# Kernel tuning notes

Measured on AMD Instinct MI355X. Metric: run time of the kernel, lower is better.

The kernel has to match this reference:

```python
import jax, jax.numpy as jnp
import numpy as np

DEPTH, DIM, HEADS, MLP_HID, POS_DIM, PROJ_DIM, NCLS, INP = 5, 128, 8, 256, 128, 128, 1000, 35
EPS = 1e-5

def _ln(x, g, b):
    m = x.mean(-1, keepdims=True)
    v = ((x - m) ** 2).mean(-1, keepdims=True)
    return (x - m) / jnp.sqrt(v + EPS) * g + b

def _gelu(x):
    return jax.nn.gelu(x, approximate=False)  # torch nn.GELU default (erf)

def setup_inputs() -> dict:
    key = jax.random.key(0)
    ks = iter(jax.random.split(key, 80))
    nxt = lambda: next(ks)
    B, N = 8, 1024
    w = lambda *s: (jax.random.normal(nxt(), s, jnp.float32) / np.sqrt(s[-2]).astype(np.float32))
    z = lambda *s: jnp.zeros(s, jnp.float32)
    o = lambda *s: jnp.ones(s, jnp.float32)
    node_feat = jax.random.normal(nxt(), (B, N, 3), jnp.float32)
    a = (jax.random.uniform(nxt(), (B, N, N)) < 0.01).astype(jnp.float32)
    adj = jnp.maximum(a, a.transpose(0, 2, 1))  # symmetric 0/1 adjacency
    lapl = jax.random.normal(nxt(), (B, N, 32), jnp.float32) * 0.1
    d = dict(
        node_feat=node_feat, adj=adj, lapl=lapl,
        cls_token=jax.random.normal(nxt(), (1, 1, DIM), jnp.float32),
        pe_w1=w(INP, 2 * INP), pe_b1=z(2 * INP),
        pe_w2=w(2 * INP, 2 * INP), pe_b2=z(2 * INP),
        pe_w3=w(2 * INP, 2 * INP), pe_b3=z(2 * INP),
        pe_lng=o(2 * INP), pe_lnb=z(2 * INP),
        pe_w4=w(2 * INP, POS_DIM), pe_b4=z(POS_DIM),
        blk_ln1_g=o(DEPTH, DIM), blk_ln1_b=z(DEPTH, DIM),
        blk_qkv_w=w(DEPTH, DIM, 3 * HEADS * DIM),
        blk_proj_w=w(DEPTH, HEADS * DIM, DIM), blk_proj_b=z(DEPTH, DIM),
        blk_gamma_w=jax.random.uniform(nxt(), (DEPTH, DIM, 2), jnp.float32) * 0.01,
        blk_gamma_b=z(DEPTH, 2),
        blk_ln2_g=o(DEPTH, DIM), blk_ln2_b=z(DEPTH, DIM),
        blk_mlp_w1=w(DEPTH, DIM, MLP_HID), blk_mlp_b1=z(DEPTH, MLP_HID),
        blk_mlp_w2=w(DEPTH, MLP_HID, DIM), blk_mlp_b2=z(DEPTH, DIM),
        head_lng=o(DIM), head_lnb=z(DIM), head_w=w(DIM, DIM), head_b=z(DIM),
        proj_w1=w(DIM, PROJ_DIM), proj_b1=z(PROJ_DIM),
        proj_w2=w(PROJ_DIM, PROJ_DIM), proj_b2=z(PROJ_DIM),
        proj_w3=w(PROJ_DIM, PROJ_DIM), proj_b3=z(PROJ_DIM),
        proj_lng=o(PROJ_DIM), proj_lnb=z(PROJ_DIM),
        proj_w4=w(PROJ_DIM, NCLS), proj_b4=z(NCLS),
    )
    return d

def reference(node_feat, adj, lapl, cls_token, pe_w1, pe_b1, pe_w2, pe_b2, pe_w3, pe_b3,
              pe_lng, pe_lnb, pe_w4, pe_b4, blk_ln1_g, blk_ln1_b, blk_qkv_w, blk_proj_w,
              blk_proj_b, blk_gamma_w, blk_gamma_b, blk_ln2_g, blk_ln2_b, blk_mlp_w1,
              blk_mlp_b1, blk_mlp_w2, blk_mlp_b2, head_lng, head_lnb, head_w, head_b,
              proj_w1, proj_b1, proj_w2, proj_b2, proj_w3, proj_b3, proj_lng, proj_lnb,
              proj_w4, proj_b4):
    B, N, _ = node_feat.shape
    M = N + 1
    # positional-encoding MLP on concatenated [node_feat | lapl] (inp_dim = 35)
    x = jnp.concatenate([node_feat, lapl], axis=2)
    x = _gelu(x @ pe_w1 + pe_b1)
    x = _gelu(x @ pe_w2 + pe_b2)
    x = _gelu(x @ pe_w3 + pe_b3)
    x = _ln(x, pe_lng, pe_lnb) @ pe_w4 + pe_b4  # [B,N,DIM]
    x = jnp.concatenate([jnp.broadcast_to(cls_token, (B, 1, DIM)), x], axis=1)  # [B,M,DIM]
    # adjacency with cls row/col, adj_cls[:,0,0] = 1
    adj_cls = jnp.zeros((B, M, M), x.dtype).at[:, 0, 0].set(1.0).at[:, 1:, 1:].set(adj)
    scale = DIM ** (-0.5)
    for i in range(DEPTH):
        h = _ln(x, blk_ln1_g[i], blk_ln1_b[i])
        qkv = (h @ blk_qkv_w[i]).reshape(B, M, 3, HEADS, DIM).transpose(2, 0, 3, 1, 4)
        q, k, v = qkv[0], qkv[1], qkv[2]  # each [B,H,M,D]
        attn = jnp.einsum('bhnd,bhmd->bhnm', q, k) * scale
        gamma = jnp.exp(h @ blk_gamma_w[i] + blk_gamma_b[i])  # [B,M,2], use_exp=True
        attn = gamma[:, None, :, 0:1] * attn + gamma[:, None, :, 1:2] * adj_cls[:, None]
        attn = jax.nn.softmax(attn, axis=-1)
        o = jnp.einsum('bhnm,bhmd->bhnd', attn, v).transpose(0, 2, 1, 3).reshape(B, M, HEADS * DIM)
        x = o @ blk_proj_w[i] + blk_proj_b[i] + h  # residual from normed input (as in source)
        h2 = _ln(x, blk_ln2_g[i], blk_ln2_b[i])
        x = _gelu(h2 @ blk_mlp_w1[i] + blk_mlp_b1[i]) @ blk_mlp_w2[i] + blk_mlp_b2[i] + h2
    c = x[:, 0]
    c = _ln(c, head_lng, head_lnb) @ head_w + head_b  # mlp_head
    p = _gelu(c @ proj_w1 + proj_b1)
    p = _gelu(p @ proj_w2 + proj_b2)
    p = _gelu(p @ proj_w3 + proj_b3)
    p = _ln(p, proj_lng, proj_lnb) @ proj_w4 + proj_b4
    return (c, p)
```

## Files before the change

kernel.cpp:

```cpp
#include <hip/hip_runtime.h>
#include <hip/hip_bf16.h>
#include <math.h>

#define NB 8
#define NSEQ 1024
#define M_ 1025
#define ROWS (NB * M_)
#define DIMC 128
#define NHEADS 8
#define QKV3 3072
#define PEROWS (NB * NSEQ)
#define ACS 1088

typedef __attribute__((ext_vector_type(8))) short bf16x8;
typedef __attribute__((ext_vector_type(4))) float f32x4;

__device__ __forceinline__ float gelu_f(float x) {
  return 0.5f * x * (1.f + erff(x * 0.70710678118654752440f));
}

__device__ __forceinline__ unsigned short f2bf(float f) {
  __hip_bfloat16 h = __float2bfloat16(f);
  return *reinterpret_cast<unsigned short*>(&h);
}

__device__ __forceinline__ float bf2f(unsigned short u) {
  union { unsigned int i; float f; } c;
  c.i = ((unsigned int)u) << 16;
  return c.f;
}

__global__ __launch_bounds__(128) void pe_fused_k(
    const float* __restrict__ nf, const float* __restrict__ lp,
    const float* __restrict__ w1, const float* __restrict__ b1,
    const float* __restrict__ w2, const float* __restrict__ b2,
    const float* __restrict__ w3, const float* __restrict__ b3,
    const float* __restrict__ lng, const float* __restrict__ lnb,
    const float* __restrict__ w4, const float* __restrict__ b4,
    float* __restrict__ x)
{
  __shared__ float sA[16][36];
  __shared__ float sB[16][72];
  __shared__ float sC[16][72];
  const int tid = threadIdx.x;
  const int r0 = blockIdx.x * 16;

  for (int i = tid; i < 16 * 35; i += 128) {
    const int r = i / 35, c = i - r * 35;
    const int gr = r0 + r;
    sA[r][c] = (c < 3) ? nf[(size_t)gr * 3 + c] : lp[(size_t)gr * 32 + (c - 3)];
  }
  __syncthreads();
  if (tid < 70) {
    float acc[16];
#pragma unroll
    for (int r = 0; r < 16; ++r) acc[r] = b1[tid];
    for (int k = 0; k < 35; ++k) {
      const float wv = w1[k * 70 + tid];
#pragma unroll
      for (int r = 0; r < 16; ++r) acc[r] = fmaf(sA[r][k], wv, acc[r]);
    }
#pragma unroll
    for (int r = 0; r < 16; ++r) sB[r][tid] = gelu_f(acc[r]);
  }
  __syncthreads();
  if (tid < 70) {
    float acc[16];
#pragma unroll
    for (int r = 0; r < 16; ++r) acc[r] = b2[tid];
    for (int k = 0; k < 70; ++k) {
      const float wv = w2[k * 70 + tid];
#pragma unroll
      for (int r = 0; r < 16; ++r) acc[r] = fmaf(sB[r][k], wv, acc[r]);
    }
#pragma unroll
    for (int r = 0; r < 16; ++r) sC[r][tid] = gelu_f(acc[r]);
  }
  __syncthreads();
  if (tid < 70) {
    float acc[16];
#pragma unroll
    for (int r = 0; r < 16; ++r) acc[r] = b3[tid];
    for (int k = 0; k < 70; ++k) {
      const float wv = w3[k * 70 + tid];
#pragma unroll
      for (int r = 0; r < 16; ++r) acc[r] = fmaf(sC[r][k], wv, acc[r]);
    }
#pragma unroll
    for (int r = 0; r < 16; ++r) sB[r][tid] = gelu_f(acc[r]);
  }
  __syncthreads();
  if (tid < 16) {
    float m = 0.f;
    for (int d = 0; d < 70; ++d) m += sB[tid][d];
    m *= (1.f / 70.f);
    float v = 0.f;
    for (int d = 0; d < 70; ++d) { const float t = sB[tid][d] - m; v += t * t; }
    const float inv = rsqrtf(v * (1.f / 70.f) + 1e-5f);
    for (int d = 0; d < 70; ++d) sB[tid][d] = (sB[tid][d] - m) * inv * lng[d] + lnb[d];
  }
  __syncthreads();
  {
    float acc[16];
#pragma unroll
    for (int r = 0; r < 16; ++r) acc[r] = b4[tid];
    for (int k = 0; k < 70; ++k) {
      const float wv = w4[k * 128 + tid];
#pragma unroll
      for (int r = 0; r < 16; ++r) acc[r] = fmaf(sB[r][k], wv, acc[r]);
    }
#pragma unroll
    for (int r = 0; r < 16; ++r) {
      const int gr = r0 + r;
      x[(size_t)(gr + gr / 1024 + 1) * DIMC + tid] = acc[r];
    }
  }
}

template<int ACT, int OBF, int RES>
__global__ __launch_bounds__(256) void mgemm_k(
    const unsigned short* __restrict__ Xb, const unsigned short* __restrict__ Wt,
    const float* __restrict__ bias, const float* __restrict__ res,
    void* __restrict__ outp, int rows, int K, int N)
{
  __shared__ unsigned short sX[64][72];
  __shared__ unsigned short sW[64][72];
  const int tid = threadIdx.x;
  const int w = tid >> 6, lane = tid & 63;
  const int col = lane & 15, quad = lane >> 4;
  const int r0 = blockIdx.x * 64, n0 = blockIdx.y * 64;
  const int lr = tid >> 2, lc = tid & 3;
  const int xrow = min(r0 + lr, rows - 1);
  const unsigned short* xsrc = Xb + (size_t)xrow * K + lc * 8;
  const unsigned short* wsrc = Wt + (size_t)(n0 + lr) * K + lc * 8;

  f32x4 acc[4];
#pragma unroll
  for (int t = 0; t < 4; ++t) acc[t] = (f32x4){0.f, 0.f, 0.f, 0.f};

  for (int k0 = 0; k0 < K; k0 += 64) {
    __syncthreads();
    *(uint4*)&sX[lr][lc * 8]      = *(const uint4*)(xsrc + k0);
    *(uint4*)&sX[lr][lc * 8 + 32] = *(const uint4*)(xsrc + k0 + 32);
    *(uint4*)&sW[lr][lc * 8]      = *(const uint4*)(wsrc + k0);
    *(uint4*)&sW[lr][lc * 8 + 32] = *(const uint4*)(wsrc + k0 + 32);
    __syncthreads();
    const bf16x8 aX0 = *(const bf16x8*)&sX[w * 16 + col][quad * 8];
    const bf16x8 aX1 = *(const bf16x8*)&sX[w * 16 + col][32 + quad * 8];
#pragma unroll
    for (int t = 0; t < 4; ++t) {
      const bf16x8 bW0 = *(const bf16x8*)&sW[t * 16 + col][quad * 8];
      const bf16x8 bW1 = *(const bf16x8*)&sW[t * 16 + col][32 + quad * 8];
      acc[t] = __builtin_amdgcn_mfma_f32_16x16x32_bf16(aX0, bW0, acc[t], 0, 0, 0);
      acc[t] = __builtin_amdgcn_mfma_f32_16x16x32_bf16(aX1, bW1, acc[t], 0, 0, 0);
    }
  }
  const int gr_base = r0 + w * 16 + quad * 4;
#pragma unroll
  for (int t = 0; t < 4; ++t) {
    const int n = n0 + t * 16 + col;
    const float bv = bias ? bias[n] : 0.f;
#pragma unroll
    for (int r = 0; r < 4; ++r) {
      const int gr = gr_base + r;
      if (gr < rows) {
        float v = acc[t][r] + bv;
        if (ACT) v = gelu_f(v);
        if (RES) v += res[(size_t)gr * N + n];
        if (OBF) ((unsigned short*)outp)[(size_t)gr * N + n] = f2bf(v);
        else     ((float*)outp)[(size_t)gr * N + n] = v;
      }
    }
  }
}

template<int OBF, int VT>
__global__ __launch_bounds__(256) void mgemm128_k(
    const unsigned short* __restrict__ Xb, const unsigned short* __restrict__ Wt,
    const float* __restrict__ bias, void* __restrict__ outp,
    unsigned short* __restrict__ vtp, int rows, int K, int N)
{
  __shared__ unsigned short sX[128][72];
  __shared__ unsigned short sW[128][72];
  const int tid = threadIdx.x;
  const int w = tid >> 6, lane = tid & 63;
  const int col = lane & 15, quad = lane >> 4;
  const int wr = w >> 1, wc = w & 1;
  const int r0 = blockIdx.x * 128, n0 = blockIdx.y * 128;

  f32x4 acc[4][4];
#pragma unroll
  for (int i = 0; i < 4; ++i)
#pragma unroll
    for (int j = 0; j < 4; ++j) acc[i][j] = (f32x4){0.f, 0.f, 0.f, 0.f};

  for (int k0 = 0; k0 < K; k0 += 64) {
    __syncthreads();
#pragma unroll
    for (int l = 0; l < 4; ++l) {
      const int idx = l * 256 + tid;
      const int row = idx >> 3, c = idx & 7;
      const int xrow = min(r0 + row, rows - 1);
      *(uint4*)&sX[row][c * 8] = *(const uint4*)(Xb + (size_t)xrow * K + k0 + c * 8);
      *(uint4*)&sW[row][c * 8] = *(const uint4*)(Wt + (size_t)(n0 + row) * K + k0 + c * 8);
    }
    __syncthreads();
    bf16x8 aX[4][2];
#pragma unroll
    for (int i = 0; i < 4; ++i) {
      aX[i][0] = *(const bf16x8*)&sX[wr * 64 + i * 16 + col][quad * 8];
      aX[i][1] = *(const bf16x8*)&sX[wr * 64 + i * 16 + col][32 + quad * 8];
    }
#pragma unroll
    for (int j = 0; j < 4; ++j) {
      const bf16x8 b0 = *(const bf16x8*)&sW[wc * 64 + j * 16 + col][quad * 8];
      const bf16x8 b1 = *(const bf16x8*)&sW[wc * 64 + j * 16 + col][32 + quad * 8];
#pragma unroll
      for (int i = 0; i < 4; ++i) {
        acc[i][j] = __builtin_amdgcn_mfma_f32_16x16x32_bf16(aX[i][0], b0, acc[i][j], 0, 0, 0);
        acc[i][j] = __builtin_amdgcn_mfma_f32_16x16x32_bf16(aX[i][1], b1, acc[i][j], 0, 0, 0);
      }
    }
  }
  const bool dovt = VT && (n0 >= 2048);
#pragma unroll
  for (int i = 0; i < 4; ++i) {
    const int gr_base = r0 + wr * 64 + i * 16 + quad * 4;
    int bb[4], mm[4];
    if (dovt) {
#pragma unroll
      for (int r = 0; r < 4; ++r) {
        const int gr = gr_base + r;
        bb[r] = gr / 1025;
        mm[r] = gr - bb[r] * 1025;
      }
    }
#pragma unroll
    for (int j = 0; j < 4; ++j) {
      const int n = n0 + wc * 64 + j * 16 + col;
      const float bv = bias ? bias[n] : 0.f;
      const int hh = (n - 2048) >> 7;
      const int d  = (n - 2048) & 127;
#pragma unroll
      for (int r = 0; r < 4; ++r) {
        const int gr = gr_base + r;
        if (gr < rows) {
          const float v = acc[i][j][r] + bv;
          const unsigned short bf = f2bf(v);
          if (OBF) ((unsigned short*)outp)[(size_t)gr * N + n] = bf;
          else     ((float*)outp)[(size_t)gr * N + n] = v;
          if (dovt) vtp[(((size_t)(bb[r] * NHEADS + hh) * DIMC + d) * ACS) + mm[r]] = bf;
        }
      }
    }
  }
}

__global__ __launch_bounds__(256) void ln_rows_k(
    const float* __restrict__ in, float* __restrict__ out,
    unsigned short* __restrict__ outb,
    const float* __restrict__ g, const float* __restrict__ b,
    const float* __restrict__ gw, const float* __restrict__ gb,
    float* __restrict__ gamout, int rows, int D)
{
  const int wv = (blockIdx.x * blockDim.x + threadIdx.x) >> 6;
  const int lane = threadIdx.x & 63;
  if (wv >= rows) return;
  const float* r = in + (size_t)wv * D;
  float s = 0.f;
  for (int d = lane; d < D; d += 64) s += r[d];
  for (int off = 32; off; off >>= 1) s += __shfl_down(s, off);
  const float mean = __shfl(s, 0) / (float)D;
  float v = 0.f;
  for (int d = lane; d < D; d += 64) { float t = r[d] - mean; v += t * t; }
  for (int off = 32; off; off >>= 1) v += __shfl_down(v, off);
  const float inv = rsqrtf(__shfl(v, 0) / (float)D + 1e-5f);
  float* orow = out + (size_t)wv * D;
  float a0 = 0.f, a1 = 0.f;
  for (int d = lane; d < D; d += 64) {
    const float o = (r[d] - mean) * inv * g[d] + b[d];
    orow[d] = o;
    if (outb) outb[(size_t)wv * D + d] = f2bf(o);
    if (gw) { a0 = fmaf(o, gw[2 * d], a0); a1 = fmaf(o, gw[2 * d + 1], a1); }
  }
  if (gw) {
    for (int off = 32; off; off >>= 1) { a0 += __shfl_down(a0, off); a1 += __shfl_down(a1, off); }
    if (lane == 0) {
      gamout[(size_t)wv * 2 + 0] = expf(a0 + gb[0]);
      gamout[(size_t)wv * 2 + 1] = expf(a1 + gb[1]);
    }
  }
}

__global__ __launch_bounds__(256) void adjp_k(const float* __restrict__ adj,
                                              unsigned long long* __restrict__ adjp)
{
  const int n = blockIdx.x;
  const int b = blockIdx.y;
  const int wv = threadIdx.x >> 6, lane = threadIdx.x & 63;
  for (int w = wv; w < 17; w += 4) {
    const int m = w * 64 + lane;
    float av = 0.f;
    if (n == 0) av = (m == 0) ? 1.f : 0.f;
    else if (m >= 1 && m <= NSEQ) av = adj[((size_t)b * NSEQ + (n - 1)) * NSEQ + (m - 1)];
    const unsigned long long mask = __ballot(av != 0.f);
    if (lane == 0) adjp[((size_t)b * M_ + n) * 17 + w] = mask;
  }
}

__global__ void wtrans_k(const float* __restrict__ W, unsigned short* __restrict__ Wt,
                         int K, int N)
{
  __shared__ float t[32][33];
  const int k0 = blockIdx.x * 32, n0 = blockIdx.y * 32;
  const float* Wd = W + (size_t)blockIdx.z * K * N;
  unsigned short* Wtd = Wt + (size_t)blockIdx.z * K * N;
  for (int i = threadIdx.y; i < 32; i += 8)
    t[i][threadIdx.x] = Wd[(size_t)(k0 + i) * N + n0 + threadIdx.x];
  __syncthreads();
  for (int i = threadIdx.y; i < 32; i += 8)
    Wtd[(size_t)(n0 + i) * K + k0 + threadIdx.x] = f2bf(t[threadIdx.x][i]);
}

__global__ __launch_bounds__(256) void attn_mfma_k(
    const unsigned short* __restrict__ qkv, const float* __restrict__ gamma,
    const unsigned long long* __restrict__ adjp, const unsigned short* __restrict__ vt,
    unsigned short* __restrict__ o)
{
  __shared__ unsigned short sK[64][136];
  __shared__ unsigned short sVt[128][72];
  __shared__ unsigned short sP[64][72];

  const int hh = blockIdx.x, qt = blockIdx.y, b = blockIdx.z;
  const int tid = threadIdx.x;
  const int w = tid >> 6;
  const int lane = tid & 63;
  const int col = lane & 15;
  const int quad = lane >> 4;
  const int n0 = qt * 64;
  const int qbase = n0 + w * 16;
  const float scale = 0.088388347648318447f;

  bf16x8 aQ[4];
  {
    const int qrow = min(qbase + col, 1024);
    const unsigned short* qp = qkv + ((size_t)(b * M_ + qrow)) * QKV3 + hh * DIMC + quad * 8;
#pragma unroll
    for (int c = 0; c < 4; ++c) aQ[c] = *(const bf16x8*)(qp + c * 32);
  }
  float g0[4], g1[4];
  size_t adjo[4];
#pragma unroll
  for (int r = 0; r < 4; ++r) {
    const int nc = min(qbase + quad * 4 + r, 1024);
    g0[r] = gamma[(size_t)(b * M_ + nc) * 2 + 0] * scale;
    g1[r] = gamma[(size_t)(b * M_ + nc) * 2 + 1];
    adjo[r] = ((size_t)b * M_ + nc) * 17;
  }

  float l_i[4] = {0.f, 0.f, 0.f, 0.f};
  f32x4 Oacc[8];
#pragma unroll
  for (int t = 0; t < 8; ++t) Oacc[t] = (f32x4){0.f, 0.f, 0.f, 0.f};

  const size_t vtbase = ((size_t)(b * NHEADS + hh)) * DIMC * ACS;

  for (int kt = 0; kt < 17; ++kt) {
    const int m0 = kt * 64;
    __syncthreads();
#pragma unroll
    for (int l = 0; l < 4; ++l) {
      const int idx = l * 256 + tid;
      {
        const int m = idx >> 4, c = idx & 15;
        const int gm = m0 + m;
        uint4 kv = make_uint4(0u, 0u, 0u, 0u);
        if (gm < M_) kv = *(const uint4*)(qkv + ((size_t)(b * M_ + gm)) * QKV3 + 1024 + hh * DIMC + c * 8);
        *(uint4*)&sK[m][c * 8] = kv;
      }
      {
        const int d = idx >> 3, mc = idx & 7;
        const uint4 vv = *(const uint4*)(vt + vtbase + (size_t)d * ACS + m0 + mc * 8);
        const int swc = mc ^ ((d >> 3) & 7);
        *(uint4*)&sVt[d][swc * 8] = vv;
      }
    }
    __syncthreads();

    unsigned long long mk[4];
#pragma unroll
    for (int r = 0; r < 4; ++r) mk[r] = adjp[adjo[r] + kt];

    f32x4 Sacc[4];
#pragma unroll
    for (int t = 0; t < 4; ++t) Sacc[t] = (f32x4){0.f, 0.f, 0.f, 0.f};
#pragma unroll
    for (int t = 0; t < 4; ++t) {
#pragma unroll
      for (int c = 0; c < 4; ++c) {
        const bf16x8 bK = *(const bf16x8*)&sK[t * 16 + col][c * 32 + quad * 8];
        Sacc[t] = __builtin_amdgcn_mfma_f32_16x16x32_bf16(aQ[c], bK, Sacc[t], 0, 0, 0);
      }
    }

#pragma unroll
    for (int t = 0; t < 4; ++t) {
      const int m = m0 + t * 16 + col;
      const bool mv = (m < M_);
      const int chb = t * 2 + (col >> 3);
      const int sh = t * 16 + col;
#pragma unroll
      for (int r = 0; r < 4; ++r) {
        const float bias = ((mk[r] >> sh) & 1ull) ? g1[r] : 0.f;
        const float s = fmaf(g0[r], Sacc[t][r], bias);
        const float pv = mv ? __expf(s) : 0.f;
        l_i[r] += pv;
        const int ql = w * 16 + quad * 4 + r;
        sP[ql][((chb ^ (ql & 7)) * 8) + (col & 7)] = f2bf(pv);
      }
    }

#pragma unroll
    for (int ch = 0; ch < 2; ++ch) {
      const int r0a = w * 16 + col;
      const bf16x8 aP = *(const bf16x8*)&sP[r0a][(((ch * 4 + quad) ^ (col & 7)) * 8)];
#pragma unroll
      for (int t = 0; t < 8; ++t) {
        const int pc = (ch * 4 + quad) ^ ((t * 2 + (col >> 3)) & 7);
        const bf16x8 bV = *(const bf16x8*)&sVt[t * 16 + col][pc * 8];
        Oacc[t] = __builtin_amdgcn_mfma_f32_16x16x32_bf16(aP, bV, Oacc[t], 0, 0, 0);
      }
    }
  }

#pragma unroll
  for (int r = 0; r < 4; ++r) {
    float s = l_i[r];
    s += __shfl_xor(s, 1);
    s += __shfl_xor(s, 2);
    s += __shfl_xor(s, 4);
    s += __shfl_xor(s, 8);
    const int n = qbase + quad * 4 + r;
    if (n < M_) {
      const float invl = 1.f / s;
      unsigned short* orow = o + ((size_t)(b * M_ + n)) * (NHEADS * DIMC) + hh * DIMC + col;
#pragma unroll
      for (int t = 0; t < 8; ++t) orow[t * 16] = f2bf(Oacc[t][r] * invl);
    }
  }
}

__global__ __launch_bounds__(256) void head_fused_k(
    const float* __restrict__ x,
    const float* __restrict__ hlg, const float* __restrict__ hlb,
    const float* __restrict__ hw, const float* __restrict__ hb,
    const float* __restrict__ pw1, const float* __restrict__ pb1,
    const float* __restrict__ pw2, const float* __restrict__ pb2,
    const float* __restrict__ pw3, const float* __restrict__ pb3,
    const float* __restrict__ plg, const float* __restrict__ plb,
    const float* __restrict__ pw4, const float* __restrict__ pb4,
    float* __restrict__ out_c, float* __restrict__ out_p)
{
  __shared__ float sA[8][128];
  __shared__ float sB[8][128];
  const int tid = threadIdx.x;

  for (int i = tid; i < 8 * 128; i += 256) {
    const int bb = i >> 7, d = i & 127;
    sA[bb][d] = x[(size_t)bb * M_ * DIMC + d];
  }
  __syncthreads();
  if (tid < 8) {
    float m = 0.f;
    for (int d = 0; d < 128; ++d) m += sA[tid][d];
    m *= (1.f / 128.f);
    float v = 0.f;
    for (int d = 0; d < 128; ++d) { const float t = sA[tid][d] - m; v += t * t; }
    const float inv = rsqrtf(v * (1.f / 128.f) + 1e-5f);
    for (int d = 0; d < 128; ++d) sA[tid][d] = (sA[tid][d] - m) * inv * hlg[d] + hlb[d];
  }
  __syncthreads();
  {
    const int j = tid & 127, rb = (tid >> 7) * 4;
    float acc[4];
#pragma unroll
    for (int r = 0; r < 4; ++r) acc[r] = hb[j];
    for (int k = 0; k < 128; ++k) {
      const float wv = hw[k * 128 + j];
#pragma unroll
      for (int r = 0; r < 4; ++r) acc[r] = fmaf(sA[rb + r][k], wv, acc[r]);
    }
#pragma unroll
    for (int r = 0; r < 4; ++r) { sB[rb + r][j] = acc[r]; out_c[(rb + r) * 128 + j] = acc[r]; }
  }
  __syncthreads();
  const float* Ws[3] = {pw1, pw2, pw3};
  const float* Bs[3] = {pb1, pb2, pb3};
  for (int s = 0; s < 3; ++s) {
    const float (*src)[128] = (s & 1) ? sA : sB;
    float (*dst)[128] = (s & 1) ? sB : sA;
    const int j = tid & 127, rb = (tid >> 7) * 4;
    float acc[4];
#pragma unroll
    for (int r = 0; r < 4; ++r) acc[r] = Bs[s][j];
    for (int k = 0; k < 128; ++k) {
      const float wv = Ws[s][k * 128 + j];
#pragma unroll
      for (int r = 0; r < 4; ++r) acc[r] = fmaf(src[rb + r][k], wv, acc[r]);
    }
#pragma unroll
    for (int r = 0; r < 4; ++r) dst[rb + r][j] = gelu_f(acc[r]);
    __syncthreads();
  }
  if (tid < 8) {
    float m = 0.f;
    for (int d = 0; d < 128; ++d) m += sA[tid][d];
    m *= (1.f / 128.f);
    float v = 0.f;
    for (int d = 0; d < 128; ++d) { const float t = sA[tid][d] - m; v += t * t; }
    const float inv = rsqrtf(v * (1.f / 128.f) + 1e-5f);
    for (int d = 0; d < 128; ++d) sA[tid][d] = (sA[tid][d] - m) * inv * plg[d] + plb[d];
  }
  __syncthreads();
  for (int j = tid; j < 1000; j += 256) {
    float acc[8];
#pragma unroll
    for (int bb = 0; bb < 8; ++bb) acc[bb] = pb4[j];
    for (int k = 0; k < 128; ++k) {
      const float wv = pw4[(size_t)k * 1000 + j];
#pragma unroll
      for (int bb = 0; bb < 8; ++bb) acc[bb] = fmaf(sA[bb][k], wv, acc[bb]);
    }
#pragma unroll
    for (int bb = 0; bb < 8; ++bb) out_p[bb * 1000 + j] = acc[bb];
  }
}

__global__ void fill_cls_k(const float* __restrict__ cls, float* __restrict__ x)
{
  x[(size_t)blockIdx.x * M_ * DIMC + threadIdx.x] = cls[threadIdx.x];
}

extern "C" void kernel_launch(void* const* d_in, const int* in_sizes, int n_in,
                              void* d_out, int out_size, void* d_ws, size_t ws_size,
                              hipStream_t stream)
{
  (void)in_sizes; (void)n_in; (void)out_size; (void)ws_size;
  const float* node_feat = (const float*)d_in[0];
  const float* adj       = (const float*)d_in[1];
  const float* lapl      = (const float*)d_in[2];
  const float* cls_token = (const float*)d_in[3];
  const float* pe_w1 = (const float*)d_in[4];
  const float* pe_b1 = (const float*)d_in[5];
  const float* pe_w2 = (const float*)d_in[6];
  const float* pe_b2 = (const float*)d_in[7];
  const float* pe_w3 = (const float*)d_in[8];
  const float* pe_b3 = (const float*)d_in[9];
  const float* pe_lng = (const float*)d_in[10];
  const float* pe_lnb = (const float*)d_in[11];
  const float* pe_w4 = (const float*)d_in[12];
  const float* pe_b4 = (const float*)d_in[13];
  const float* blk_ln1_g = (const float*)d_in[14];
  const float* blk_ln1_b = (const float*)d_in[15];
  const float* blk_qkv_w = (const float*)d_in[16];
  const float* blk_proj_w = (const float*)d_in[17];
  const float* blk_proj_b = (const float*)d_in[18];
  const float* blk_gamma_w = (const float*)d_in[19];
  const float* blk_gamma_b = (const float*)d_in[20];
  const float* blk_ln2_g = (const float*)d_in[21];
  const float* blk_ln2_b = (const float*)d_in[22];
  const float* blk_mlp_w1 = (const float*)d_in[23];
  const float* blk_mlp_b1 = (const float*)d_in[24];
  const float* blk_mlp_w2 = (const float*)d_in[25];
  const float* blk_mlp_b2 = (const float*)d_in[26];
  const float* head_lng = (const float*)d_in[27];
  const float* head_lnb = (const float*)d_in[28];
  const float* head_w = (const float*)d_in[29];
  const float* head_b = (const float*)d_in[30];
  const float* proj_w1 = (const float*)d_in[31];
  const float* proj_b1 = (const float*)d_in[32];
  const float* proj_w2 = (const float*)d_in[33];
  const float* proj_b2 = (const float*)d_in[34];
  const float* proj_w3 = (const float*)d_in[35];
  const float* proj_b3 = (const float*)d_in[36];
  const float* proj_lng = (const float*)d_in[37];
  const float* proj_lnb = (const float*)d_in[38];
  const float* proj_w4 = (const float*)d_in[39];
  const float* proj_b4 = (const float*)d_in[40];

  float* ws   = (float*)d_ws;
  float* x    = ws;
  float* h    = x + 1049600;
  float* gam  = h + 1049600;
  float* obuf = gam + 16400;
  unsigned short* obufb = (unsigned short*)obuf;
  unsigned short* hidb  = (unsigned short*)(obuf + 4198400);
  float* sm  = obuf + 5248000;
  unsigned short* hb   = (unsigned short*)(sm + 8192);
  unsigned short* qkv  = hb + 1049600;
  unsigned long long* adjp = (unsigned long long*)(qkv + 25190400);
  unsigned short* vt   = (unsigned short*)(adjp + 139400 + 88);
  unsigned short* qkvWt = vt + 8912896;
  unsigned short* projWt = qkvWt + 5 * 393216;
  unsigned short* mlp1Wt = projWt + 5 * 131072;
  unsigned short* mlp2Wt = mlp1Wt + 5 * 32768;

  float* out_c = (float*)d_out;
  float* out_p = out_c + NB * DIMC;

  adjp_k<<<dim3(M_, NB), 256, 0, stream>>>(adj, adjp);
  wtrans_k<<<dim3(4, 96, 5), dim3(32, 8), 0, stream>>>(blk_qkv_w, qkvWt, 128, 3072);
  wtrans_k<<<dim3(32, 4, 5), dim3(32, 8), 0, stream>>>(blk_proj_w, projWt, 1024, 128);
  wtrans_k<<<dim3(4, 8, 5), dim3(32, 8), 0, stream>>>(blk_mlp_w1, mlp1Wt, 128, 256);
  wtrans_k<<<dim3(8, 4, 5), dim3(32, 8), 0, stream>>>(blk_mlp_w2, mlp2Wt, 256, 128);

  pe_fused_k<<<512, 128, 0, stream>>>(node_feat, lapl, pe_w1, pe_b1, pe_w2, pe_b2,
                                      pe_w3, pe_b3, pe_lng, pe_lnb, pe_w4, pe_b4, x);
  fill_cls_k<<<NB, DIMC, 0, stream>>>(cls_token, x);

  const int lnGrid = (ROWS * 64 + 255) / 256;
  for (int i = 0; i < 5; ++i) {
    const float* ln1g = blk_ln1_g + i * DIMC;
    const float* ln1b = blk_ln1_b + i * DIMC;
    const float* pb   = blk_proj_b + i * DIMC;
    const float* gw   = blk_gamma_w + (size_t)i * DIMC * 2;
    const float* gb   = blk_gamma_b + i * 2;
    const float* ln2g = blk_ln2_g + i * DIMC;
    const float* ln2b = blk_ln2_b + i * DIMC;
    const float* mb1  = blk_mlp_b1 + i * 256;
    const float* mb2  = blk_mlp_b2 + i * DIMC;
    const unsigned short* qw = qkvWt + (size_t)i * 393216;
    const unsigned short* pw = projWt + (size_t)i * 131072;
    const unsigned short* m1w = mlp1Wt + (size_t)i * 32768;
    const unsigned short* m2w = mlp2Wt + (size_t)i * 32768;

    ln_rows_k<<<lnGrid, 256, 0, stream>>>(x, h, hb, ln1g, ln1b, gw, gb, gam, ROWS, DIMC);
    mgemm128_k<1, 1><<<dim3(65, 24), 256, 0, stream>>>(hb, qw, nullptr, qkv, vt, ROWS, 128, 3072);
    attn_mfma_k<<<dim3(NHEADS, 17, NB), 256, 0, stream>>>(qkv, gam, adjp, vt, obufb);
    mgemm_k<0, 0, 1><<<dim3(129, 2), 256, 0, stream>>>(obufb, pw, pb, h, x, ROWS, 1024, 128);
    ln_rows_k<<<lnGrid, 256, 0, stream>>>(x, h, hb, ln2g, ln2b, nullptr, nullptr, nullptr, ROWS, DIMC);
    mgemm_k<1, 1, 0><<<dim3(129, 4), 256, 0, stream>>>(hb, m1w, mb1, nullptr, hidb, ROWS, 128, 256);
    mgemm_k<0, 0, 1><<<dim3(129, 2), 256, 0, stream>>>(hidb, m2w, mb2, h, x, ROWS, 256, 128);
  }

  head_fused_k<<<1, 256, 0, stream>>>(x, head_lng, head_lnb, head_w, head_b,
                                      proj_w1, proj_b1, proj_w2, proj_b2,
                                      proj_w3, proj_b3, proj_lng, proj_lnb,
                                      proj_w4, proj_b4, out_c, out_p);
}
```

Baseline: 1.593 ms.

## Fuse LayerNorms into the following QKV and MLP1 GEMM prologues

Removes the standalone LayerNorm kernels by computing LN1 (plus the gamma projection and exp) inside the QKV GEMM, and LN2 inside a new MLP1 GEMM kernel. Normalized rows are written as bf16 straight into shared memory, and only the first column-block writes the fp32 residual copy and gamma. This drops two launches per layer and the hb round trip. In exchange each of the 24 QKV column blocks and 4 MLP1 blocks recomputes the LayerNorm for its rows, and the register-heavy prologue (64 floats per thread) may lower occupancy.

```diff
diff --git a/kernel.cpp b/kernel.cpp
--- a/kernel.cpp
+++ b/kernel.cpp
@@ -174,13 +174,15 @@
   }
 }
 
-template<int OBF, int VT>
-__global__ __launch_bounds__(256) void mgemm128_k(
-    const unsigned short* __restrict__ Xb, const unsigned short* __restrict__ Wt,
-    const float* __restrict__ bias, void* __restrict__ outp,
-    unsigned short* __restrict__ vtp, int rows, int K, int N)
-{
-  __shared__ unsigned short sX[128][72];
+__global__ __launch_bounds__(256) void ln1qkv_k(
+    const float* __restrict__ x,
+    const float* __restrict__ g, const float* __restrict__ b,
+    const float* __restrict__ gw, const float* __restrict__ gb,
+    const unsigned short* __restrict__ Wt,
+    unsigned short* __restrict__ qkvp, unsigned short* __restrict__ vtp,
+    float* __restrict__ h, float* __restrict__ gam)
+{
+  __shared__ unsigned short sX[128][136];
   __shared__ unsigned short sW[128][72];
   const int tid = threadIdx.x;
   const int w = tid >> 6, lane = tid & 63;
@@ -188,28 +190,75 @@
   const int wr = w >> 1, wc = w & 1;
   const int r0 = blockIdx.x * 128, n0 = blockIdx.y * 128;
 
+  {
+    const int r = tid >> 1, half = tid & 1;
+    const int gr = min(r0 + r, ROWS - 1);
+    const float* xr = x + (size_t)gr * DIMC + half * 64;
+    float v[64];
+    float s = 0.f;
+#pragma unroll
+    for (int i = 0; i < 64; i += 4) {
+      const float4 f = *(const float4*)(xr + i);
+      v[i] = f.x; v[i+1] = f.y; v[i+2] = f.z; v[i+3] = f.w;
+      s += f.x + f.y + f.z + f.w;
+    }
+    s += __shfl_xor(s, 1);
+    const float mean = s * (1.f / 128.f);
+    float ss = 0.f;
+#pragma unroll
+    for (int i = 0; i < 64; ++i) { const float t = v[i] - mean; ss += t * t; }
+    ss += __shfl_xor(ss, 1);
+    const float inv = rsqrtf(ss * (1.f / 128.f) + 1e-5f);
+    float a0 = 0.f, a1 = 0.f;
+#pragma unroll
+    for (int i = 0; i < 64; ++i) {
+      const int c = half * 64 + i;
+      const float o = (v[i] - mean) * inv * g[c] + b[c];
+      v[i] = o;
+      a0 = fmaf(o, gw[2 * c], a0);
+      a1 = fmaf(o, gw[2 * c + 1], a1);
+    }
+    unsigned int packed[32];
+#pragma unroll
+    for (int i = 0; i < 32; ++i)
+      packed[i] = (unsigned int)f2bf(v[2 * i]) | ((unsigned int)f2bf(v[2 * i + 1]) << 16);
+#pragma unroll
+    for (int i = 0; i < 8; ++i)
+      *(uint4*)&sX[r][half * 64 + i * 8] = *(uint4*)&packed[i * 4];
+    a0 += __shfl_xor(a0, 1);
+    a1 += __shfl_xor(a1, 1);
+    if (blockIdx.y == 0 && r0 + r < ROWS) {
+      float* hr = h + (size_t)gr * DIMC + half * 64;
+#pragma unroll
+      for (int i = 0; i < 64; i += 4)
+        *(float4*)(hr + i) = make_float4(v[i], v[i+1], v[i+2], v[i+3]);
+      if (half == 0) {
+        gam[(size_t)gr * 2 + 0] = expf(a0 + gb[0]);
+        gam[(size_t)gr * 2 + 1] = expf(a1 + gb[1]);
+      }
+    }
+  }
+
   f32x4 acc[4][4];
 #pragma unroll
   for (int i = 0; i < 4; ++i)
 #pragma unroll
     for (int j = 0; j < 4; ++j) acc[i][j] = (f32x4){0.f, 0.f, 0.f, 0.f};
 
-  for (int k0 = 0; k0 < K; k0 += 64) {
+  for (int k0 = 0; k0 < 128; k0 += 64) {
     __syncthreads();
 #pragma unroll
     for (int l = 0; l < 4; ++l) {
       const int idx = l * 256 + tid;
       const int row = idx >> 3, c = idx & 7;
-      const int xrow = min(r0 + row, rows - 1);
-      *(uint4*)&sX[row][c * 8] = *(const uint4*)(Xb + (size_t)xrow * K + k0 + c * 8);
-      *(uint4*)&sW[row][c * 8] = *(const uint4*)(Wt + (size_t)(n0 + row) * K + k0 + c * 8);
+      *(uint4*)&sW[row][c * 8] = *(const uint4*)(Wt + (size_t)(n0 + row) * 128 + k0 + c * 8);
     }
     __syncthreads();
     bf16x8 aX[4][2];
 #pragma unroll
     for (int i = 0; i < 4; ++i) {
-      aX[i][0] = *(const bf16x8*)&sX[wr * 64 + i * 16 + col][quad * 8];
-      aX[i][1] = *(const bf16x8*)&sX[wr * 64 + i * 16 + col][32 + quad * 8];
+      aX[i][0] = *(const bf16x8*)&sX[wr * 64 + i * 16 + col][k0 + quad * 8];
+      aX[i][1] = *(const bf16x8*)&sX[wr * 64 + i * 16 + col][k0 + 32 + quad * 8];
     }
 #pragma unroll
     for (int j = 0; j < 4; ++j) {
@@ -222,7 +271,7 @@
       }
     }
   }
-  const bool dovt = VT && (n0 >= 2048);
+  const bool dovt = (n0 >= 2048);
 #pragma unroll
   for (int i = 0; i < 4; ++i) {
     const int gr_base = r0 + wr * 64 + i * 16 + quad * 4;
@@ -238,17 +287,14 @@
 #pragma unroll
     for (int j = 0; j < 4; ++j) {
       const int n = n0 + wc * 64 + j * 16 + col;
-      const float bv = bias ? bias[n] : 0.f;
       const int hh = (n - 2048) >> 7;
       const int d  = (n - 2048) & 127;
 #pragma unroll
       for (int r = 0; r < 4; ++r) {
         const int gr = gr_base + r;
-        if (gr < rows) {
-          const float v = acc[i][j][r] + bv;
-          const unsigned short bf = f2bf(v);
-          if (OBF) ((unsigned short*)outp)[(size_t)gr * N + n] = bf;
-          else     ((float*)outp)[(size_t)gr * N + n] = v;
+        if (gr < ROWS) {
+          const unsigned short bf = f2bf(acc[i][j][r]);
+          qkvp[(size_t)gr * QKV3 + n] = bf;
           if (dovt) vtp[(((size_t)(bb[r] * NHEADS + hh) * DIMC + d) * ACS) + mm[r]] = bf;
         }
       }
@@ -256,38 +302,90 @@
   }
 }
 
-__global__ __launch_bounds__(256) void ln_rows_k(
-    const float* __restrict__ in, float* __restrict__ out,
-    unsigned short* __restrict__ outb,
+__global__ __launch_bounds__(256) void ln2mlp1_k(
+    const float* __restrict__ x,
     const float* __restrict__ g, const float* __restrict__ b,
-    const float* __restrict__ gw, const float* __restrict__ gb,
-    float* __restrict__ gamout, int rows, int D)
-{
-  const int wv = (blockIdx.x * blockDim.x + threadIdx.x) >> 6;
-  const int lane = threadIdx.x & 63;
-  if (wv >= rows) return;
-  const float* r = in + (size_t)wv * D;
-  float s = 0.f;
-  for (int d = lane; d < D; d += 64) s += r[d];
-  for (int off = 32; off; off >>= 1) s += __shfl_down(s, off);
-  const float mean = __shfl(s, 0) / (float)D;
-  float v = 0.f;
-  for (int d = lane; d < D; d += 64) { float t = r[d] - mean; v += t * t; }
-  for (int off = 32; off; off >>= 1) v += __shfl_down(v, off);
-  const float inv = rsqrtf(__shfl(v, 0) / (float)D + 1e-5f);
-  float* orow = out + (size_t)wv * D;
-  float a0 = 0.f, a1 = 0.f;
-  for (int d = lane; d < D; d += 64) {
-    const float o = (r[d] - mean) * inv * g[d] + b[d];
-    orow[d] = o;
-    if (outb) outb[(size_t)wv * D + d] = f2bf(o);
-    if (gw) { a0 = fmaf(o, gw[2 * d], a0); a1 = fmaf(o, gw[2 * d + 1], a1); }
-  }
-  if (gw) {
-    for (int off = 32; off; off >>= 1) { a0 += __shfl_down(a0, off); a1 += __shfl_down(a1, off); }
-    if (lane == 0) {
-      gamout[(size_t)wv * 2 + 0] = expf(a0 + gb[0]);
-      gamout[(size_t)wv * 2 + 1] = expf(a1 + gb[1]);
+    const unsigned short* __restrict__ Wt, const float* __restrict__ bias,
+    float* __restrict__ h2, unsigned short* __restrict__ hidb)
+{
+  __shared__ unsigned short sX[64][136];
+  __shared__ unsigned short sW[64][136];
+  const int tid = threadIdx.x;
+  const int w = tid >> 6, lane = tid & 63;
+  const int col = lane & 15, quad = lane >> 4;
+  const int r0 = blockIdx.x * 64, n0 = blockIdx.y * 64;
+
+  {
+    const int wrow = tid >> 2, seg = tid & 3;
+    const unsigned short* src = Wt + (size_t)(n0 + wrow) * 128 + seg * 32;
+    *(uint4*)&sW[wrow][seg * 32]      = *(const uint4*)(src);
+    *(uint4*)&sW[wrow][seg * 32 + 8]  = *(const uint4*)(src + 8);
+    *(uint4*)&sW[wrow][seg * 32 + 16] = *(const uint4*)(src + 16);
+    *(uint4*)&sW[wrow][seg * 32 + 24] = *(const uint4*)(src + 24);
+  }
+  {
+    const int r = tid >> 2, seg = tid & 3;
+    const int gr = min(r0 + r, ROWS - 1);
+    const float* xr = x + (size_t)gr * DIMC + seg * 32;
+    float v[32];
+    float s = 0.f;
+#pragma unroll
+    for (int i = 0; i < 32; i += 4) {
+      const float4 f = *(const float4*)(xr + i);
+      v[i] = f.x; v[i+1] = f.y; v[i+2] = f.z; v[i+3] = f.w;
+      s += f.x + f.y + f.z + f.w;
+    }
+    s += __shfl_xor(s, 1);
+    s += __shfl_xor(s, 2);
+    const float mean = s * (1.f / 128.f);
+    float ss = 0.f;
+#pragma unroll
+    for (int i = 0; i < 32; ++i) { const float t = v[i] - mean; ss += t * t; }
+    ss += __shfl_xor(ss, 1);
+    ss += __shfl_xor(ss, 2);
+    const float inv = rsqrtf(ss * (1.f / 128.f) + 1e-5f);
+#pragma unroll
+    for (int i = 0; i < 32; ++i) {
+      const int c = seg * 32 + i;
+      v[i] = (v[i] - mean) * inv * g[c] + b[c];
+    }
+    unsigned int packed[16];
+#pragma unroll
+    for (int i = 0; i < 16; ++i)
+      packed[i] = (unsigned int)f2bf(v[2 * i]) | ((unsigned int)f2bf(v[2 * i + 1]) << 16);
+#pragma unroll
+    for (int i = 0; i < 4; ++i)
+      *(uint4*)&sX[r][seg * 32 + i * 8] = *(uint4*)&packed[i * 4];
+    if (blockIdx.y == 0 && r0 + r < ROWS) {
+      float* hr = h2 + (size_t)gr * DIMC + seg * 32;
+#pragma unroll
+      for (int i = 0; i < 32; i += 4)
+        *(float4*)(hr + i) = make_float4(v[i], v[i+1], v[i+2], v[i+3]);
+    }
+  }
+  __syncthreads();
+
+  f32x4 acc[4];
+#pragma unroll
+  for (int t = 0; t < 4; ++t) acc[t] = (f32x4){0.f, 0.f, 0.f, 0.f};
+#pragma unroll
+  for (int kc = 0; kc < 4; ++kc) {
+    const bf16x8 aX = *(const bf16x8*)&sX[w * 16 + col][kc * 32 + quad * 8];
+#pragma unroll
+    for (int t = 0; t < 4; ++t) {
+      const bf16x8 bW = *(const bf16x8*)&sW[t * 16 + col][kc * 32 + quad * 8];
+      acc[t] = __builtin_amdgcn_mfma_f32_16x16x32_bf16(aX, bW, acc[t], 0, 0, 0);
+    }
+  }
+  const int gr_base = r0 + w * 16 + quad * 4;
+#pragma unroll
+  for (int t = 0; t < 4; ++t) {
+    const int n = n0 + t * 16 + col;
+    const float bv = bias[n];
+#pragma unroll
+    for (int r = 0; r < 4; ++r) {
+      const int gr = gr_base + r;
+      if (gr < ROWS) hidb[(size_t)gr * 256 + n] = f2bf(gelu_f(acc[t][r] + bv));
     }
   }
 }
@@ -618,7 +716,6 @@
                                       pe_w3, pe_b3, pe_lng, pe_lnb, pe_w4, pe_b4, x);
   fill_cls_k<<<NB, DIMC, 0, stream>>>(cls_token, x);
 
-  const int lnGrid = (ROWS * 64 + 255) / 256;
   for (int i = 0; i < 5; ++i) {
     const float* ln1g = blk_ln1_g + i * DIMC;
     const float* ln1b = blk_ln1_b + i * DIMC;
@@ -634,12 +731,10 @@
     const unsigned short* m1w = mlp1Wt + (size_t)i * 32768;
     const unsigned short* m2w = mlp2Wt + (size_t)i * 32768;
 
-    ln_rows_k<<<lnGrid, 256, 0, stream>>>(x, h, hb, ln1g, ln1b, gw, gb, gam, ROWS, DIMC);
-    mgemm128_k<1, 1><<<dim3(65, 24), 256, 0, stream>>>(hb, qw, nullptr, qkv, vt, ROWS, 128, 3072);
+    ln1qkv_k<<<dim3(65, 24), 256, 0, stream>>>(x, ln1g, ln1b, gw, gb, qw, qkv, vt, h, gam);
     attn_mfma_k<<<dim3(NHEADS, 17, NB), 256, 0, stream>>>(qkv, gam, adjp, vt, obufb);
     mgemm_k<0, 0, 1><<<dim3(129, 2), 256, 0, stream>>>(obufb, pw, pb, h, x, ROWS, 1024, 128);
-    ln_rows_k<<<lnGrid, 256, 0, stream>>>(x, h, hb, ln2g, ln2b, nullptr, nullptr, nullptr, ROWS, DIMC);
-    mgemm_k<1, 1, 0><<<dim3(129, 4), 256, 0, stream>>>(hb, m1w, mb1, nullptr, hidb, ROWS, 128, 256);
+    ln2mlp1_k<<<dim3(129, 4), 256, 0, stream>>>(x, ln2g, ln2b, m1w, mb1, h, hidb);
     mgemm_k<0, 0, 1><<<dim3(129, 2), 256, 0, stream>>>(hidb, m2w, mb2, h, x, ROWS, 256, 128);
   }
 
```

After: 1.756 ms. 10.2% more time.
